# Performance work log

Hardware: AMD Instinct MI355X
Metric: run time of the kernel (lower is better)

Reference implementation:

```python
import jax, jax.numpy as jnp
import numpy as np

B, L, F = 256, 512, 64
NUM_IDS = 2000
LN_EPS = 1e-5


def setup_inputs() -> dict:
    key = jax.random.key(0)
    ks = jax.random.split(key, 16)
    s = 0.05
    return {
        # padded neighbor-id sequences; 0 is the padding id
        "src_ids": jax.random.randint(ks[0], (B, L), 0, NUM_IDS, dtype=jnp.int64)
        if jax.config.jax_enable_x64 else jax.random.randint(ks[0], (B, L), 0, NUM_IDS, dtype=jnp.int32),
        "dst_ids": jax.random.randint(ks[1], (B, L), 0, NUM_IDS, dtype=jnp.int64)
        if jax.config.jax_enable_x64 else jax.random.randint(ks[1], (B, L), 0, NUM_IDS, dtype=jnp.int32),
        # co-occurrence encode MLP: Linear(1->F), ReLU, Linear(F->F)
        "enc_w1": jax.random.normal(ks[2], (1, F), jnp.float32) * s,
        "enc_b1": jax.random.normal(ks[3], (F,), jnp.float32) * s,
        "enc_w2": jax.random.normal(ks[4], (F, F), jnp.float32) * s,
        "enc_b2": jax.random.normal(ks[5], (F,), jnp.float32) * s,
        # cross-attention projections (bias-free q/k/v as in source)
        "Wq": jax.random.normal(ks[6], (F, F), jnp.float32) * s,
        "Wk": jax.random.normal(ks[7], (F, F), jnp.float32) * s,
        "Wv": jax.random.normal(ks[8], (F, F), jnp.float32) * s,
        "Wo": jax.random.normal(ks[9], (F, F), jnp.float32) * s,
        "bo": jax.random.normal(ks[10], (F,), jnp.float32) * s,
        "ln_g": jnp.ones((F,), jnp.float32),
        "ln_b": jnp.zeros((F,), jnp.float32),
    }


def _counts_in(a, b):
    # for each element of a: how many times does it occur in b (same batch row)
    # equivalent to the np.unique count / mapping-dict lookup in the original
    return (a[:, :, None] == b[:, None, :]).sum(axis=-1).astype(jnp.float32)


def _appearances(a, b):
    # [B, L, 2]: counts of each id of `a` in (a, b); zero out padding (id==0)
    app = jnp.stack([_counts_in(a, a), _counts_in(a, b)], axis=-1)
    return jnp.where((a == 0)[..., None], 0.0, app)


def _encode(app, w1, b1, w2, b2):
    # Linear(1->F) -> ReLU -> Linear(F->F), then sum over the 2 count channels
    h = jax.nn.relu(app[..., None] * w1[0] + b1)  # [B, L, 2, F]
    h = jnp.einsum('blcf,fg->blcg', h, w2) + b2
    return h.sum(axis=2)  # [B, L, F]


def _linear_attn(q, k, v):
    dim = q.shape[-1]
    q = jax.nn.softmax(q, axis=-1) * (dim ** -0.5)
    k = jax.nn.softmax(k, axis=1)  # softmax over sequence dim (dim=-2)
    ctx = jnp.einsum('bld,ble->bde', k, v)
    return jnp.einsum('bld,bde->ble', q, ctx)


def _layer_norm(x, g, b):
    mu = x.mean(axis=-1, keepdims=True)
    var = ((x - mu) ** 2).mean(axis=-1, keepdims=True)
    return (x - mu) * jax.lax.rsqrt(var + LN_EPS) * g + b


def _cross_attn(x, ctx, Wq, Wk, Wv, Wo, bo, ln_g, ln_b):
    q, k, v = x @ Wq, ctx @ Wk, ctx @ Wv
    attn = _linear_attn(q, k, v)
    return _layer_norm(x + attn @ Wo + bo, ln_g, ln_b)


def reference(src_ids, dst_ids, enc_w1, enc_b1, enc_w2, enc_b2,
              Wq, Wk, Wv, Wo, bo, ln_g, ln_b):
    # neighbor co-occurrence counting + encoding
    src_app = _appearances(src_ids, dst_ids)  # [B, L, 2]
    dst_app = _appearances(dst_ids, src_ids)
    src_feat = _encode(src_app, enc_w1, enc_b1, enc_w2, enc_b2)  # [B, L, F]
    dst_feat = _encode(dst_app, enc_w1, enc_b1, enc_w2, enc_b2)
    # linear cross-attention fusion (shared weights, both directions)
    src_out = _cross_attn(src_feat, dst_feat, Wq, Wk, Wv, Wo, bo, ln_g, ln_b)
    dst_out = _cross_attn(dst_feat, src_feat, Wq, Wk, Wv, Wo, bo, ln_g, ln_b)
    return jnp.stack([src_out, dst_out])  # [2, B, L, F]
```

## Files before the change

### kernel.cpp

```cpp
#include <hip/hip_runtime.h>
#include <hip/hip_bf16.h>

#define BB 256
#define LL 512

typedef float nfloat4 __attribute__((ext_vector_type(4)));

__global__ __launch_bounds__(256, 2) void k_all(
    const int* __restrict__ src, const int* __restrict__ dst,
    const float* __restrict__ w1, const float* __restrict__ b1,
    const float* __restrict__ w2, const float* __restrict__ b2,
    const float* __restrict__ Wq, const float* __restrict__ Wk,
    const float* __restrict__ Wv, const float* __restrict__ Wo,
    const float* __restrict__ bo, const float* __restrict__ lng,
    const float* __restrict__ lnb, float* __restrict__ out) {
  __shared__ __align__(16) char smem[63776];
  int*   hist  = (int*)smem;
  float* poolF = (float*)smem;
  int*   hkey  = (int*)(smem + 16384);
  int*   hmult = (int*)(smem + 20480);
  float* tabL  = (float*)(smem + 16384);
  float* Mg    = (float*)(smem + 32768);
  int*   xkey  = (int*)(smem + 50176);
  int*   ckey  = (int*)(smem + 52224);
  int*   cmult = (int*)(smem + 54272);
  int*   pidxl = (int*)(smem + 56320);
  int*   cflag = (int*)(smem + 58368);
  int*   clist = (int*)(smem + 60424);
  float* fbF   = (float*)(smem + 60688);
  int*   npp   = (int*)(smem + 63760);

  int bd = blockIdx.x, b = bd >> 1, dir = bd & 1;
  int tid = threadIdx.x, tx = tid & 63, ty = tid >> 6;
  int e0 = ty * 16;

  const int* s = src + b * LL;
  const int* d = dst + b * LL;
  int sid0 = s[tid], sid1 = s[tid + 256];
  int did0 = d[tid], did1 = d[tid + 256];
  for (int i = tid; i < 4000; i += 256) hist[i] = 0;
  for (int i = tid; i < 1024; i += 256) { hkey[i] = -1; hmult[i] = 0; }
  for (int i = tid; i < 513; i += 256) cflag[i] = 0;
  if (tid < 3) npp[tid] = 0;
  __syncthreads();

  atomicAdd(&hist[sid0], 1);        atomicAdd(&hist[sid1], 1);
  atomicAdd(&hist[2000 + did0], 1); atomicAdd(&hist[2000 + did1], 1);
  __syncthreads();

  int x0 = dir ? did0 : sid0, x1 = dir ? did1 : sid1;
  int c0 = dir ? sid0 : did0, c1 = dir ? sid1 : did1;
  const int* hx = dir ? hist + 2000 : hist;
  const int* hc = dir ? hist : hist + 2000;

  int slot0 = 0, slot1 = 0;
#pragma unroll
  for (int r = 0; r < 4; ++r) {
    int side = r >> 1;
    int id = (r == 0) ? c0 : (r == 1) ? c1 : (r == 2) ? x0 : x1;
    int ca = 0, cb = 0;
    if (id != 0) {
      if (side == 0) { ca = hc[id]; cb = hx[id]; }
      else           { ca = hx[id]; cb = hc[id]; }
    }
    int key = ca | (cb << 10) | (side << 20);
    int h = (int)(((unsigned)key * 2654435761u) >> 22) & 1023;
    while (true) {
      int old = atomicCAS(&hkey[h], -1, key);
      if (old == -1 || old == key) break;
      h = (h + 1) & 1023;
    }
    if (side == 0) atomicAdd(&hmult[h], 1);
    else if (r == 2) slot0 = h;
    else slot1 = h;
  }
  __syncthreads();

  for (int i = tid; i < 1024; i += 256) {
    int k = hkey[i];
    if (k != -1) {
      if (k & (1 << 20)) {
        int idx = atomicAdd(&npp[1], 1);
        xkey[idx] = k & 0xFFFFF;
        hkey[i] = idx;
      } else {
        int idx = atomicAdd(&npp[0], 1);
        ckey[idx]  = k;
        cmult[idx] = hmult[i];
      }
    }
  }
  __syncthreads();
  int Pc = npp[0], Px = npp[1];
  pidxl[tid]       = hkey[slot0];
  pidxl[tid + 256] = hkey[slot1];
  for (int i = tid; i < Pc; i += 256) { int k = ckey[i]; cflag[k & 1023] = 1; cflag[k >> 10] = 1; }
  for (int i = tid; i < Px; i += 256) { int k = xkey[i]; cflag[k & 1023] = 1; cflag[k >> 10] = 1; }
  __syncthreads();
  for (int c = tid; c < 513; c += 256) {
    if (cflag[c]) {
      int idx = atomicAdd(&npp[2], 1);
      clist[idx] = c;
      cflag[c] = idx;
    }
  }
  __syncthreads();
  int nc = npp[2];
  for (int i = tid; i < Pc; i += 256) { int k = ckey[i]; ckey[i] = cflag[k & 1023] | (cflag[k >> 10] << 10); }
  for (int i = tid; i < Px; i += 256) { int k = xkey[i]; xkey[i] = cflag[k & 1023] | (cflag[k >> 10] << 10); }

  float wcA[64], wcB[64];
#pragma unroll
  for (int f = 0; f < 64; ++f) wcA[f] = w2[f * 64 + tx];
  {
    float w1v = w1[tx], b1v = b1[tx], b2v = b2[tx];
    for (int i = ty; i < nc; i += 4) {
      float c = (float)clist[i];
      fbF[ty * 64 + tx] = fmaxf(c * w1v + b1v, 0.f);
      float acc = b2v;
      const float4* h4 = (const float4*)&fbF[ty * 64];
#pragma unroll
      for (int q = 0; q < 16; ++q) {
        float4 hv = h4[q];
        acc += hv.x * wcA[4 * q] + hv.y * wcA[4 * q + 1] + hv.z * wcA[4 * q + 2] + hv.w * wcA[4 * q + 3];
      }
      tabL[i * 64 + tx] = acc;
    }
  }
#pragma unroll
  for (int f = 0; f < 64; ++f) { wcA[f] = Wk[f * 64 + tx]; wcB[f] = Wv[f * 64 + tx]; }
  float macc[16];
#pragma unroll
  for (int e = 0; e < 16; ++e) macc[e] = 0.f;
  float sacc = 0.f;
  __syncthreads();

  float* pA = poolF;
  float* vA = poolF + 2048;
  for (int j0 = 0; j0 < Pc; j0 += 32) {
    int cN = min(32, Pc - j0);
    for (int j = ty; j < cN; j += 4) {
      int key = ckey[j0 + j];
      int ia = key & 1023, ib = key >> 10;
      fbF[ty * 64 + tx] = tabL[ia * 64 + tx] + tabL[ib * 64 + tx];
      float kr = 0.f, vr = 0.f;
      const float4* fb4 = (const float4*)&fbF[ty * 64];
#pragma unroll
      for (int q = 0; q < 16; ++q) {
        float4 fv = fb4[q];
        kr += fv.x * wcA[4 * q] + fv.y * wcA[4 * q + 1] + fv.z * wcA[4 * q + 2] + fv.w * wcA[4 * q + 3];
        vr += fv.x * wcB[4 * q] + fv.y * wcB[4 * q + 1] + fv.z * wcB[4 * q + 2] + fv.w * wcB[4 * q + 3];
      }
      float p = __expf(kr) * (float)cmult[j0 + j];
      sacc += p;
      pA[j * 64 + tx] = p;
      vA[j * 64 + tx] = vr;
    }
    __syncthreads();
    for (int jj = 0; jj < cN; ++jj) {
      float pg = pA[jj * 64 + tx];
      const float4* vb4 = (const float4*)&vA[jj * 64 + e0];
#pragma unroll
      for (int q = 0; q < 4; ++q) {
        float4 vv = vb4[q];
        macc[4 * q]     += pg * vv.x; macc[4 * q + 1] += pg * vv.y;
        macc[4 * q + 2] += pg * vv.z; macc[4 * q + 3] += pg * vv.w;
      }
    }
    __syncthreads();
  }
  fbF[512 + ty * 64 + tx] = sacc;
  __syncthreads();
  float inv = 1.f / (fbF[512 + tx] + fbF[576 + tx] + fbF[640 + tx] + fbF[704 + tx]);
#pragma unroll
  for (int e = 0; e < 16; ++e) Mg[(e0 + e) * 68 + tx] = macc[e] * inv;
  for (int i = tid; i < 4096; i += 256) poolF[i] = Wo[i];
#pragma unroll
  for (int f = 0; f < 64; ++f) wcA[f] = Wq[f * 64 + tx];
  float bov = bo[tx], lg = lng[tx], lb = lnb[tx];
  __syncthreads();

#pragma unroll
  for (int e = 0; e < 16; ++e) macc[e] = 0.f;
  for (int f = 0; f < 64; ++f) {
    float mt = Mg[f * 68 + tx];
    const float4* wo4 = (const float4*)&poolF[f * 64 + e0];
#pragma unroll
    for (int q = 0; q < 4; ++q) {
      float4 w4 = wo4[q];
      macc[4 * q]     += mt * w4.x; macc[4 * q + 1] += mt * w4.y;
      macc[4 * q + 2] += mt * w4.z; macc[4 * q + 3] += mt * w4.w;
    }
  }
  __syncthreads();
#pragma unroll
  for (int e = 0; e < 16; ++e) Mg[(e0 + e) * 68 + tx] = macc[e];
  __syncthreads();

  for (int i0 = 0; i0 < Px; i0 += 64) {
    int cN = min(64, Px - i0);
    for (int jj = ty; jj < cN; jj += 4) {
      int key = xkey[i0 + jj];
      int ia = key & 1023, ib = key >> 10;
      float fv = tabL[ia * 64 + tx] + tabL[ib * 64 + tx];
      fbF[ty * 64 + tx] = fv;
      float qr = 0.f;
      const float4* fb4 = (const float4*)&fbF[ty * 64];
#pragma unroll
      for (int q = 0; q < 16; ++q) {
        float4 f4v = fb4[q];
        qr += f4v.x * wcA[4 * q] + f4v.y * wcA[4 * q + 1] + f4v.z * wcA[4 * q + 2] + f4v.w * wcA[4 * q + 3];
      }
      float p = __expf(qr);
      float sum = p;
#pragma unroll
      for (int off = 32; off >= 1; off >>= 1) sum += __shfl_xor(sum, off, 64);
      float qh = p / sum * 0.125f;
      fbF[256 + ty * 64 + tx] = qh;
      float at = 0.f;
      const float4* qb4 = (const float4*)&fbF[256 + ty * 64];
      const float4* gt4 = (const float4*)&Mg[tx * 68];
#pragma unroll
      for (int q = 0; q < 16; ++q) {
        float4 qv = qb4[q];
        float4 gv = gt4[q];
        at += qv.x * gv.x + qv.y * gv.y + qv.z * gv.z + qv.w * gv.w;
      }
      float r = fv + at + bov;
      float mu = r;
#pragma unroll
      for (int off = 32; off >= 1; off >>= 1) mu += __shfl_xor(mu, off, 64);
      mu *= (1.f / 64.f);
      float dv = r - mu;
      float var = dv * dv;
#pragma unroll
      for (int off = 32; off >= 1; off >>= 1) var += __shfl_xor(var, off, 64);
      var *= (1.f / 64.f);
      poolF[jj * 64 + tx] = dv * rsqrtf(var + 1e-5f) * lg + lb;
    }
    __syncthreads();
    const nfloat4* w4 = (const nfloat4*)poolF;
    nfloat4* out4 = (nfloat4*)(out + (size_t)(dir * BB + b) * (LL * 64));
    for (int idx = tid; idx < 512 * 16; idx += 256) {
      int l = idx >> 4, q = idx & 15;
      int pid = pidxl[l];
      if (pid >= i0 && pid < i0 + cN)
        __builtin_nontemporal_store(w4[(pid - i0) * 16 + q], &out4[l * 16 + q]);
    }
    __syncthreads();
  }
}

extern "C" void kernel_launch(void* const* d_in, const int* in_sizes, int n_in,
                              void* d_out, int out_size, void* d_ws, size_t ws_size,
                              hipStream_t stream) {
  const int* src  = (const int*)d_in[0];
  const int* dst  = (const int*)d_in[1];
  const float* w1 = (const float*)d_in[2];
  const float* b1 = (const float*)d_in[3];
  const float* w2 = (const float*)d_in[4];
  const float* b2 = (const float*)d_in[5];
  const float* Wq = (const float*)d_in[6];
  const float* Wk = (const float*)d_in[7];
  const float* Wv = (const float*)d_in[8];
  const float* Wo = (const float*)d_in[9];
  const float* bo = (const float*)d_in[10];
  const float* lng = (const float*)d_in[11];
  const float* lnb = (const float*)d_in[12];
  float* out = (float*)d_out;

  k_all<<<dim3(512), dim3(256), 0, stream>>>(src, dst, w1, b1, w2, b2,
                                             Wq, Wk, Wv, Wo, bo, lng, lnb, out);
}
```

Measured before the change: 119.9 us.

## Pack src/dst histograms into one array and apply Wo per row instead of prefolding

```diff
diff --git a/kernel.cpp b/kernel.cpp
--- a/kernel.cpp
+++ b/kernel.cpp
@@ -1,5 +1,4 @@
 #include <hip/hip_runtime.h>
-#include <hip/hip_bf16.h>
 
 #define BB 256
 #define LL 512
@@ -38,20 +37,24 @@
   const int* d = dst + b * LL;
   int sid0 = s[tid], sid1 = s[tid + 256];
   int did0 = d[tid], did1 = d[tid + 256];
-  for (int i = tid; i < 4000; i += 256) hist[i] = 0;
+
+  float wcA[64], wcB[64];
+#pragma unroll
+  for (int f = 0; f < 64; ++f) wcA[f] = w2[f * 64 + tx];
+  float w1v = w1[tx], b1v = b1[tx], b2v = b2[tx];
+
+  for (int i = tid; i < 2000; i += 256) hist[i] = 0;
   for (int i = tid; i < 1024; i += 256) { hkey[i] = -1; hmult[i] = 0; }
   for (int i = tid; i < 513; i += 256) cflag[i] = 0;
   if (tid < 3) npp[tid] = 0;
   __syncthreads();
 
-  atomicAdd(&hist[sid0], 1);        atomicAdd(&hist[sid1], 1);
-  atomicAdd(&hist[2000 + did0], 1); atomicAdd(&hist[2000 + did1], 1);
+  atomicAdd(&hist[sid0], 1);      atomicAdd(&hist[sid1], 1);
+  atomicAdd(&hist[did0], 65536);  atomicAdd(&hist[did1], 65536);
   __syncthreads();
 
   int x0 = dir ? did0 : sid0, x1 = dir ? did1 : sid1;
   int c0 = dir ? sid0 : did0, c1 = dir ? sid1 : did1;
-  const int* hx = dir ? hist + 2000 : hist;
-  const int* hc = dir ? hist : hist + 2000;
 
   int slot0 = 0, slot1 = 0;
 #pragma unroll
@@ -60,8 +63,10 @@
     int id = (r == 0) ? c0 : (r == 1) ? c1 : (r == 2) ? x0 : x1;
     int ca = 0, cb = 0;
     if (id != 0) {
-      if (side == 0) { ca = hc[id]; cb = hx[id]; }
-      else           { ca = hx[id]; cb = hc[id]; }
+      int hv = hist[id];
+      int cs = hv & 0xffff, cd2 = hv >> 16;
+      if (side != dir) { ca = cs; cb = cd2; }
+      else             { ca = cd2; cb = cs; }
     }
     int key = ca | (cb << 10) | (side << 20);
     int h = (int)(((unsigned)key * 2654435761u) >> 22) & 1023;
@@ -109,23 +114,17 @@
   for (int i = tid; i < Pc; i += 256) { int k = ckey[i]; ckey[i] = cflag[k & 1023] | (cflag[k >> 10] << 10); }
   for (int i = tid; i < Px; i += 256) { int k = xkey[i]; xkey[i] = cflag[k & 1023] | (cflag[k >> 10] << 10); }
 
-  float wcA[64], wcB[64];
-#pragma unroll
-  for (int f = 0; f < 64; ++f) wcA[f] = w2[f * 64 + tx];
-  {
-    float w1v = w1[tx], b1v = b1[tx], b2v = b2[tx];
-    for (int i = ty; i < nc; i += 4) {
-      float c = (float)clist[i];
-      fbF[ty * 64 + tx] = fmaxf(c * w1v + b1v, 0.f);
-      float acc = b2v;
-      const float4* h4 = (const float4*)&fbF[ty * 64];
-#pragma unroll
-      for (int q = 0; q < 16; ++q) {
-        float4 hv = h4[q];
-        acc += hv.x * wcA[4 * q] + hv.y * wcA[4 * q + 1] + hv.z * wcA[4 * q + 2] + hv.w * wcA[4 * q + 3];
-      }
-      tabL[i * 64 + tx] = acc;
-    }
+  for (int i = ty; i < nc; i += 4) {
+    float c = (float)clist[i];
+    fbF[ty * 64 + tx] = fmaxf(c * w1v + b1v, 0.f);
+    float acc = b2v;
+    const float4* h4 = (const float4*)&fbF[ty * 64];
+#pragma unroll
+    for (int q = 0; q < 16; ++q) {
+      float4 hv = h4[q];
+      acc += hv.x * wcA[4 * q] + hv.y * wcA[4 * q + 1] + hv.z * wcA[4 * q + 2] + hv.w * wcA[4 * q + 3];
+    }
+    tabL[i * 64 + tx] = acc;
   }
 #pragma unroll
   for (int f = 0; f < 64; ++f) { wcA[f] = Wk[f * 64 + tx]; wcB[f] = Wv[f * 64 + tx]; }
@@ -156,6 +155,7 @@
       pA[j * 64 + tx] = p;
       vA[j * 64 + tx] = vr;
     }
+    if (j0 + 32 >= Pc) fbF[512 + ty * 64 + tx] = sacc;
     __syncthreads();
     for (int jj = 0; jj < cN; ++jj) {
       float pg = pA[jj * 64 + tx];
@@ -169,32 +169,12 @@
     }
     __syncthreads();
   }
-  fbF[512 + ty * 64 + tx] = sacc;
-  __syncthreads();
   float inv = 1.f / (fbF[512 + tx] + fbF[576 + tx] + fbF[640 + tx] + fbF[704 + tx]);
 #pragma unroll
   for (int e = 0; e < 16; ++e) Mg[(e0 + e) * 68 + tx] = macc[e] * inv;
-  for (int i = tid; i < 4096; i += 256) poolF[i] = Wo[i];
-#pragma unroll
-  for (int f = 0; f < 64; ++f) wcA[f] = Wq[f * 64 + tx];
+#pragma unroll
+  for (int f = 0; f < 64; ++f) { wcA[f] = Wq[f * 64 + tx]; wcB[f] = Wo[f * 64 + tx]; }
   float bov = bo[tx], lg = lng[tx], lb = lnb[tx];
-  __syncthreads();
-
-#pragma unroll
-  for (int e = 0; e < 16; ++e) macc[e] = 0.f;
-  for (int f = 0; f < 64; ++f) {
-    float mt = Mg[f * 68 + tx];
-    const float4* wo4 = (const float4*)&poolF[f * 64 + e0];
-#pragma unroll
-    for (int q = 0; q < 4; ++q) {
-      float4 w4 = wo4[q];
-      macc[4 * q]     += mt * w4.x; macc[4 * q + 1] += mt * w4.y;
-      macc[4 * q + 2] += mt * w4.z; macc[4 * q + 3] += mt * w4.w;
-    }
-  }
-  __syncthreads();
-#pragma unroll
-  for (int e = 0; e < 16; ++e) Mg[(e0 + e) * 68 + tx] = macc[e];
   __syncthreads();
 
   for (int i0 = 0; i0 < Px; i0 += 64) {
@@ -217,14 +197,22 @@
       for (int off = 32; off >= 1; off >>= 1) sum += __shfl_xor(sum, off, 64);
       float qh = p / sum * 0.125f;
       fbF[256 + ty * 64 + tx] = qh;
+      float t = 0.f;
+      const float4* qb4 = (const float4*)&fbF[256 + ty * 64];
+      const float4* mt4 = (const float4*)&Mg[tx * 68];
+#pragma unroll
+      for (int q = 0; q < 16; ++q) {
+        float4 qv = qb4[q];
+        float4 mv = mt4[q];
+        t += qv.x * mv.x + qv.y * mv.y + qv.z * mv.z + qv.w * mv.w;
+      }
+      fbF[512 + ty * 64 + tx] = t;
       float at = 0.f;
-      const float4* qb4 = (const float4*)&fbF[256 + ty * 64];
-      const float4* gt4 = (const float4*)&Mg[tx * 68];
-#pragma unroll
-      for (int q = 0; q < 16; ++q) {
-        float4 qv = qb4[q];
-        float4 gv = gt4[q];
-        at += qv.x * gv.x + qv.y * gv.y + qv.z * gv.z + qv.w * gv.w;
+      const float4* tb4 = (const float4*)&fbF[512 + ty * 64];
+#pragma unroll
+      for (int q = 0; q < 16; ++q) {
+        float4 tv = tb4[q];
+        at += tv.x * wcB[4 * q] + tv.y * wcB[4 * q + 1] + tv.z * wcB[4 * q + 2] + tv.w * wcB[4 * q + 3];
       }
       float r = fv + at + bov;
       float mu = r;
```

New measurement: 117.9 us. No clear change (-1.7%).
